# Performance work log

Hardware: AMD Instinct MI355X
Metric: run time of the kernel (lower is better)

## Reference

```python
import jax, jax.numpy as jnp
import numpy as np
import math

D_MODEL = 768
NUM_HEADS = 12
SPARSITY = 0.7


def setup_inputs() -> dict:
    key = jax.random.key(0)
    ks = jax.random.split(key, 9)
    B, S, D = 2, 2048, D_MODEL
    scale = 1.0 / math.sqrt(D)  # xavier-ish
    inp = {
        "x": jax.random.normal(ks[0], (B, S, D), dtype=jnp.float32),
        "Wq": jax.random.normal(ks[1], (D, D), dtype=jnp.float32) * scale,
        "bq": jnp.zeros((D,), dtype=jnp.float32),
        "Wk": jax.random.normal(ks[2], (D, D), dtype=jnp.float32) * scale,
        "bk": jnp.zeros((D,), dtype=jnp.float32),
        "Wv": jax.random.normal(ks[3], (D, D), dtype=jnp.float32) * scale,
        "bv": jnp.zeros((D,), dtype=jnp.float32),
        "Wo": jax.random.normal(ks[4], (D, D), dtype=jnp.float32) * scale,
        "bo": jnp.zeros((D,), dtype=jnp.float32),
    }
    return inp


def reference(x, Wq, bq, Wk, bk, Wv, bv, Wo, bo):
    B, S, D = x.shape
    H = NUM_HEADS
    hd = D // H
    k_keep = max(1, int((1.0 - SPARSITY) * S))

    # projections (nn.Linear: x @ W.T + b), split into heads -> [B,H,S,hd]
    q = (x @ Wq.T + bq).reshape(B, S, H, hd).transpose(0, 2, 1, 3)
    k = (x @ Wk.T + bk).reshape(B, S, H, hd).transpose(0, 2, 1, 3)
    v = (x @ Wv.T + bv).reshape(B, S, H, hd).transpose(0, 2, 1, 3)

    # dense scores [B,H,S,S]
    scores = jnp.einsum("bhqd,bhkd->bhqk", q, k) / math.sqrt(hd)

    # per-row top-k sparsification (training path of the torch module)
    _, topk_idx = jax.lax.top_k(scores, k_keep)  # [B,H,S,k]
    bi = jnp.arange(B)[:, None, None, None]
    hi = jnp.arange(H)[None, :, None, None]
    si = jnp.arange(S)[None, None, :, None]
    keep = jnp.zeros(scores.shape, dtype=bool).at[bi, hi, si, topk_idx].set(True)
    scores = jnp.where(keep, scores, jnp.float32(-1e9))

    attn = jax.nn.softmax(scores, axis=-1)
    out = jnp.einsum("bhqk,bhkd->bhqd", attn, v)  # [B,H,S,hd]
    out = out.transpose(0, 2, 1, 3).reshape(B, S, D)
    return out @ Wo.T + bo
```

## Files before the change

kernel.cpp:

```cpp
#include <hip/hip_runtime.h>
#include <math.h>

#define B_ 2
#define S_ 2048
#define D_ 768
#define H_ 12
#define HD_ 64
#define KKEEP 614
#define M_ (B_*S_)
#define KD_ 768
#define SRW 2072

typedef __attribute__((ext_vector_type(8))) short bf8;
typedef __attribute__((ext_vector_type(4))) float f4;

__device__ __forceinline__ unsigned short f2bf(float f) {
    unsigned u = __float_as_uint(f);
    u += 0x7FFF + ((u >> 16) & 1);
    return (unsigned short)(u >> 16);
}
__device__ __forceinline__ float bf2f(unsigned short h) {
    return __uint_as_float((unsigned)h << 16);
}
__device__ __forceinline__ unsigned f2ord16(float f) {
    unsigned u = __float_as_uint(f);
    unsigned o32 = u ^ ((unsigned)((int)u >> 31) | 0x80000000u);
    return (o32 + 0x7FFFu + ((o32 >> 16) & 1u)) >> 16;
}
__device__ __forceinline__ float ord16_to_f(unsigned o16) {
    unsigned o = o16 << 16;
    unsigned mask = 0x80000000u | ~(unsigned)((int)o >> 31);
    return __uint_as_float((o ^ mask) & 0xFFFF0000u);
}

__global__ void split_kernel(const float* __restrict__ src,
                             unsigned short* __restrict__ hi,
                             unsigned short* __restrict__ lo, int n) {
    int i = blockIdx.x * blockDim.x + threadIdx.x;
    if (i >= n) return;
    float f = src[i];
    unsigned short h = f2bf(f);
    hi[i] = h;
    lo[i] = f2bf(f - bf2f(h));
}

__global__ void split_w_kernel(const float* __restrict__ w0, const float* __restrict__ w1,
                               const float* __restrict__ w2, const float* __restrict__ w3,
                               unsigned short* __restrict__ hi,
                               unsigned short* __restrict__ lo) {
    const int which = blockIdx.y;
    const float* src = which == 0 ? w0 : (which == 1 ? w1 : (which == 2 ? w2 : w3));
    int i = blockIdx.x * blockDim.x + threadIdx.x;
    size_t o = (size_t)which * (D_ * D_) + i;
    float f = src[i];
    unsigned short h = f2bf(f);
    hi[o] = h;
    lo[o] = f2bf(f - bf2f(h));
}

__global__ __launch_bounds__(256)
void gemm_qkv(const unsigned short* __restrict__ Ahi, const unsigned short* __restrict__ Alo,
              const unsigned short* __restrict__ Wch, const unsigned short* __restrict__ Wcl,
              const float* __restrict__ bq, const float* __restrict__ bk,
              const float* __restrict__ bv,
              unsigned short* __restrict__ Qh, unsigned short* __restrict__ Ql,
              unsigned short* __restrict__ Kh, unsigned short* __restrict__ Vth) {
    __shared__ unsigned short Ah[128][32], Al[128][32], Bh[64][32], Bl[64][32];
    const int bm = blockIdx.x * 128, bnG = blockIdx.y * 64;
    const int which = blockIdx.y / 12;
    const int bn = bnG - which * 768;
    const float* bias = which == 0 ? bq : (which == 1 ? bk : bv);
    const int tid = threadIdx.x, lane = tid & 63, wave = tid >> 6;
    const int col = lane & 15, quad = lane >> 4;

    f4 acc[2][4];
#pragma unroll
    for (int mi = 0; mi < 2; ++mi)
#pragma unroll
        for (int ni = 0; ni < 4; ++ni) { f4 z = {0.f,0.f,0.f,0.f}; acc[mi][ni] = z; }

    for (int kt = 0; kt < KD_; kt += 32) {
        __syncthreads();
#pragma unroll
        for (int c = 0; c < 2; ++c) {
            int idx = c * 256 + tid;
            int row = idx >> 2, ko = (idx & 3) * 8;
            *(uint4*)&Ah[row][ko] = *(const uint4*)&Ahi[(size_t)(bm + row) * KD_ + kt + ko];
            *(uint4*)&Al[row][ko] = *(const uint4*)&Alo[(size_t)(bm + row) * KD_ + kt + ko];
        }
        {
            int row = tid >> 2, ko = (tid & 3) * 8;
            *(uint4*)&Bh[row][ko] = *(const uint4*)&Wch[(size_t)(bnG + row) * KD_ + kt + ko];
            *(uint4*)&Bl[row][ko] = *(const uint4*)&Wcl[(size_t)(bnG + row) * KD_ + kt + ko];
        }
        __syncthreads();

        bf8 af[2][2], wf[4][2];
#pragma unroll
        for (int mi = 0; mi < 2; ++mi) {
            int r = wave * 32 + mi * 16 + col;
            af[mi][0] = *(const bf8*)&Ah[r][quad * 8];
            af[mi][1] = *(const bf8*)&Al[r][quad * 8];
        }
#pragma unroll
        for (int ni = 0; ni < 4; ++ni) {
            int r = ni * 16 + col;
            wf[ni][0] = *(const bf8*)&Bh[r][quad * 8];
            wf[ni][1] = *(const bf8*)&Bl[r][quad * 8];
        }
#pragma unroll
        for (int mi = 0; mi < 2; ++mi)
#pragma unroll
            for (int ni = 0; ni < 4; ++ni) {
                acc[mi][ni] = __builtin_amdgcn_mfma_f32_16x16x32_bf16(af[mi][0], wf[ni][0], acc[mi][ni], 0, 0, 0);
                acc[mi][ni] = __builtin_amdgcn_mfma_f32_16x16x32_bf16(af[mi][1], wf[ni][0], acc[mi][ni], 0, 0, 0);
                acc[mi][ni] = __builtin_amdgcn_mfma_f32_16x16x32_bf16(af[mi][0], wf[ni][1], acc[mi][ni], 0, 0, 0);
            }
    }

    float bvv[4];
#pragma unroll
    for (int ni = 0; ni < 4; ++ni) bvv[ni] = bias[bn + ni * 16 + col];
#pragma unroll
    for (int mi = 0; mi < 2; ++mi)
#pragma unroll
        for (int ni = 0; ni < 4; ++ni)
#pragma unroll
            for (int r = 0; r < 4; ++r) {
                int m = bm + wave * 32 + mi * 16 + quad * 4 + r;
                int n = bn + ni * 16 + col;
                float v = acc[mi][ni][r] + bvv[ni];
                if (which == 0) v *= 0.125f;
                int b = m >> 11, s = m & 2047, h = n >> 6, d = n & 63;
                unsigned short hh = f2bf(v);
                if (which == 0) {
                    size_t idx = (((size_t)b * H_ + h) * S_ + s) * HD_ + d;
                    Qh[idx] = hh;
                    Ql[idx] = f2bf(v - bf2f(hh));
                } else if (which == 1) {
                    Kh[(((size_t)b * H_ + h) * S_ + s) * HD_ + d] = hh;
                } else {
                    Vth[(((size_t)b * H_ + h) * HD_ + d) * S_ + s] = hh;
                }
            }
}

__global__ __launch_bounds__(256)
void gemm_o(const unsigned short* __restrict__ Ahi, const unsigned short* __restrict__ Alo,
            const unsigned short* __restrict__ Whi, const unsigned short* __restrict__ Wlo,
            const float* __restrict__ bias, float* __restrict__ outf) {
    __shared__ unsigned short Ah[128][32], Al[128][32], Bh[64][32], Bl[64][32];
    const int bm = blockIdx.x * 128, bn = blockIdx.y * 64;
    const int tid = threadIdx.x, lane = tid & 63, wave = tid >> 6;
    const int col = lane & 15, quad = lane >> 4;

    f4 acc[2][4];
#pragma unroll
    for (int mi = 0; mi < 2; ++mi)
#pragma unroll
        for (int ni = 0; ni < 4; ++ni) { f4 z = {0.f,0.f,0.f,0.f}; acc[mi][ni] = z; }

    for (int kt = 0; kt < KD_; kt += 32) {
        __syncthreads();
#pragma unroll
        for (int c = 0; c < 2; ++c) {
            int idx = c * 256 + tid;
            int row = idx >> 2, ko = (idx & 3) * 8;
            *(uint4*)&Ah[row][ko] = *(const uint4*)&Ahi[(size_t)(bm + row) * KD_ + kt + ko];
            *(uint4*)&Al[row][ko] = *(const uint4*)&Alo[(size_t)(bm + row) * KD_ + kt + ko];
        }
        {
            int row = tid >> 2, ko = (tid & 3) * 8;
            *(uint4*)&Bh[row][ko] = *(const uint4*)&Whi[(size_t)(bn + row) * KD_ + kt + ko];
            *(uint4*)&Bl[row][ko] = *(const uint4*)&Wlo[(size_t)(bn + row) * KD_ + kt + ko];
        }
        __syncthreads();

        bf8 af[2][2], wf[4][2];
#pragma unroll
        for (int mi = 0; mi < 2; ++mi) {
            int r = wave * 32 + mi * 16 + col;
            af[mi][0] = *(const bf8*)&Ah[r][quad * 8];
            af[mi][1] = *(const bf8*)&Al[r][quad * 8];
        }
#pragma unroll
        for (int ni = 0; ni < 4; ++ni) {
            int r = ni * 16 + col;
            wf[ni][0] = *(const bf8*)&Bh[r][quad * 8];
            wf[ni][1] = *(const bf8*)&Bl[r][quad * 8];
        }
#pragma unroll
        for (int mi = 0; mi < 2; ++mi)
#pragma unroll
            for (int ni = 0; ni < 4; ++ni) {
                acc[mi][ni] = __builtin_amdgcn_mfma_f32_16x16x32_bf16(af[mi][0], wf[ni][0], acc[mi][ni], 0, 0, 0);
                acc[mi][ni] = __builtin_amdgcn_mfma_f32_16x16x32_bf16(af[mi][1], wf[ni][0], acc[mi][ni], 0, 0, 0);
                acc[mi][ni] = __builtin_amdgcn_mfma_f32_16x16x32_bf16(af[mi][0], wf[ni][1], acc[mi][ni], 0, 0, 0);
            }
    }

    float bvv[4];
#pragma unroll
    for (int ni = 0; ni < 4; ++ni) bvv[ni] = bias[bn + ni * 16 + col];
#pragma unroll
    for (int mi = 0; mi < 2; ++mi)
#pragma unroll
        for (int ni = 0; ni < 4; ++ni)
#pragma unroll
            for (int r = 0; r < 4; ++r) {
                int m = bm + wave * 32 + mi * 16 + quad * 4 + r;
                int n = bn + ni * 16 + col;
                outf[(size_t)m * D_ + n] = acc[mi][ni][r] + bvv[ni];
            }
}

__global__ __launch_bounds__(1024, 8)
void attn_kernel(const unsigned short* __restrict__ Qhi, const unsigned short* __restrict__ Qlo,
                 const unsigned short* __restrict__ Khi,
                 const unsigned short* __restrict__ Vthi,
                 unsigned short* __restrict__ AOhi, unsigned short* __restrict__ AOlo) {
    const int bid = blockIdx.x;
    const int xcd = bid & 7, sub = (bid >> 3) % 3, tile = bid / 24;
    const int bh = xcd * 3 + sub;
    const int b = bh / H_, h = bh % H_;
    const int q0 = tile * 16;
    const int tid = threadIdx.x, lane = tid & 63, wave = tid >> 6;
    const int col = lane & 15, quad = lane >> 4;

    __shared__ __align__(16) unsigned char arena[16 * 4144];
    unsigned short* scB = (unsigned short*)arena;
    float (*osum)[16][64] = (float (*)[16][64])arena;
    __shared__ float linv[16];

    const size_t qbase = ((size_t)bh * S_ + q0 + col) * HD_;
    bf8 qh0 = *(const bf8*)&Qhi[qbase + quad * 8];
    bf8 qh1 = *(const bf8*)&Qhi[qbase + 32 + quad * 8];
    bf8 ql0 = *(const bf8*)&Qlo[qbase + quad * 8];
    bf8 ql1 = *(const bf8*)&Qlo[qbase + 32 + quad * 8];

    const size_t kbb = (size_t)bh * S_ * HD_;
#pragma unroll 1
    for (int t = 0; t < 8; ++t) {
        const size_t kr = kbb + (size_t)(wave * 128 + t * 16 + col) * HD_;
        bf8 kh0 = *(const bf8*)&Khi[kr + quad * 8];
        bf8 kh1 = *(const bf8*)&Khi[kr + 32 + quad * 8];
        f4 a = {0.f, 0.f, 0.f, 0.f};
        a = __builtin_amdgcn_mfma_f32_16x16x32_bf16(qh0, kh0, a, 0, 0, 0);
        a = __builtin_amdgcn_mfma_f32_16x16x32_bf16(qh1, kh1, a, 0, 0, 0);
        a = __builtin_amdgcn_mfma_f32_16x16x32_bf16(ql0, kh0, a, 0, 0, 0);
        a = __builtin_amdgcn_mfma_f32_16x16x32_bf16(ql1, kh1, a, 0, 0, 0);
#pragma unroll
        for (int r = 0; r < 4; ++r)
            scB[(quad * 4 + r) * SRW + wave * 128 + t * 16 + col] =
                (unsigned short)f2ord16(a[r]);
    }
    __syncthreads();

    unsigned* rowp = (unsigned*)(arena + wave * 4144);
    unsigned kv[16], kvs[16];
#pragma unroll
    for (int j = 0; j < 16; ++j) kv[j] = rowp[lane + 64 * j];
#pragma unroll
    for (int j = 0; j < 16; ++j) kvs[j] = kv[j] << 16;

    unsigned Mhi = 0, Mlo = 0;
#pragma unroll
    for (int j = 0; j < 16; ++j) {
        Mhi = kv[j]  > Mhi ? kv[j]  : Mhi;
        Mlo = kvs[j] > Mlo ? kvs[j] : Mlo;
    }
    unsigned mo = (Mhi >> 16) > (Mlo >> 16) ? (Mhi >> 16) : (Mlo >> 16);
#pragma unroll
    for (int off = 1; off < 64; off <<= 1) {
        unsigned v = __shfl_xor((int)mo, off, 64);
        mo = mo > v ? mo : v;
    }
    const float m = ord16_to_f(mo);

    unsigned T = 0;
#pragma unroll 1
    for (int bit = 15; bit >= 0; --bit) {
        unsigned candh = (T | (1u << bit)) << 16;
        int cnt = 0;
#pragma unroll
        for (int j = 0; j < 16; ++j) {
            cnt += __popcll(__ballot(kv[j]  >= candh));
            cnt += __popcll(__ballot(kvs[j] >= candh));
        }
        if (cnt >= KKEEP) T |= (1u << bit);
    }

    float ls = 0.f;
#pragma unroll 1
    for (int j = 0; j < 16; ++j) {
        unsigned lo16 = kv[j] & 0xFFFFu;
        unsigned hi16 = kv[j] >> 16;
        float wl = __expf(ord16_to_f(lo16) - m);
        float wh = __expf(ord16_to_f(hi16) - m);
        wl = (lo16 >= T) ? wl : 0.f;
        wh = (hi16 >= T) ? wh : 0.f;
        ls += wl + wh;
        rowp[lane + 64 * j] = (unsigned)f2bf(wl) | ((unsigned)f2bf(wh) << 16);
    }
#pragma unroll
    for (int off = 1; off < 64; off <<= 1) ls += __shfl_xor(ls, off, 64);
    if (lane == 0) linv[wave] = 1.f / ls;
    __syncthreads();

    f4 od[4];
#pragma unroll
    for (int dt = 0; dt < 4; ++dt) { f4 z = {0.f,0.f,0.f,0.f}; od[dt] = z; }
    const size_t vbb = (size_t)bh * HD_ * S_;
#pragma unroll 1
    for (int c = 0; c < 4; ++c) {
        bf8 ph = *(const bf8*)&scB[col * SRW + wave * 128 + c * 32 + quad * 8];
        const size_t sbase = (size_t)(wave * 128 + c * 32 + quad * 8);
#pragma unroll
        for (int dt = 0; dt < 4; ++dt) {
            bf8 vh = *(const bf8*)&Vthi[vbb + (size_t)(dt * 16 + col) * S_ + sbase];
            od[dt] = __builtin_amdgcn_mfma_f32_16x16x32_bf16(ph, vh, od[dt], 0, 0, 0);
        }
    }
    __syncthreads();
#pragma unroll
    for (int dt = 0; dt < 4; ++dt)
#pragma unroll
        for (int r = 0; r < 4; ++r)
            osum[wave][quad * 4 + r][dt * 16 + col] = od[dt][r];
    __syncthreads();

    {
        int q = tid >> 6, d = tid & 63;
        float s = 0.f;
#pragma unroll
        for (int w = 0; w < 16; ++w) s += osum[w][q][d];
        s *= linv[q];
        size_t idx = ((size_t)b * S_ + q0 + q) * D_ + h * HD_ + d;
        unsigned short hh = f2bf(s);
        AOhi[idx] = hh;
        AOlo[idx] = f2bf(s - bf2f(hh));
    }
}

extern "C" void kernel_launch(void* const* d_in, const int* in_sizes, int n_in,
                              void* d_out, int out_size, void* d_ws, size_t ws_size,
                              hipStream_t stream) {
    const float* x  = (const float*)d_in[0];
    const float* Wq = (const float*)d_in[1];
    const float* bq = (const float*)d_in[2];
    const float* Wk = (const float*)d_in[3];
    const float* bk = (const float*)d_in[4];
    const float* Wv = (const float*)d_in[5];
    const float* bv = (const float*)d_in[6];
    const float* Wo = (const float*)d_in[7];
    const float* bo = (const float*)d_in[8];
    float* out = (float*)d_out;

    const size_t NP = (size_t)M_ * D_;
    const size_t NW = (size_t)D_ * D_;
    unsigned short* p = (unsigned short*)d_ws;
    unsigned short* xhi = p;  p += NP;
    unsigned short* xlo = p;  p += NP;
    unsigned short* Wch = p;  p += 4 * NW;
    unsigned short* Wcl = p;  p += 4 * NW;
    unsigned short* Qh  = p;  p += NP;  unsigned short* Ql  = p;  p += NP;
    unsigned short* Kh  = p;  p += NP;
    unsigned short* Vth = p;  p += NP;
    unsigned short* AOh = xhi;
    unsigned short* AOl = xlo;

    split_kernel<<<(int)(NP / 256), 256, 0, stream>>>(x, xhi, xlo, (int)NP);
    {
        dim3 gw((unsigned)(NW / 256), 4);
        split_w_kernel<<<gw, 256, 0, stream>>>(Wq, Wk, Wv, Wo, Wch, Wcl);
    }

    {
        dim3 g(M_ / 128, 36);
        gemm_qkv<<<g, 256, 0, stream>>>(xhi, xlo, Wch, Wcl, bq, bk, bv,
                                        Qh, Ql, Kh, Vth);
    }

    attn_kernel<<<(S_ / 16) * B_ * H_, 1024, 0, stream>>>(Qh, Ql, Kh, Vth, AOh, AOl);

    {
        dim3 g(M_ / 128, D_ / 64);
        gemm_o<<<g, 256, 0, stream>>>(AOh, AOl, Wch + 3 * NW, Wcl + 3 * NW, bo, out);
    }
}
```

Measured before the change: 433.4 us.

## Enlarge projection GEMM tiles to 128x128 and load tiles directly into LDS

```diff
diff --git a/kernel.cpp b/kernel.cpp
--- a/kernel.cpp
+++ b/kernel.cpp
@@ -31,6 +31,13 @@
     unsigned o = o16 << 16;
     unsigned mask = 0x80000000u | ~(unsigned)((int)o >> 31);
     return __uint_as_float((o ^ mask) & 0xFFFF0000u);
+}
+
+__device__ __forceinline__ void gload16(const unsigned short* g, unsigned short* l) {
+    __builtin_amdgcn_global_load_lds(
+        (const __attribute__((address_space(1))) unsigned int*)(const void*)g,
+        (__attribute__((address_space(3))) unsigned int*)(void*)l,
+        16, 0, 0);
 }
 
 __global__ void split_kernel(const float* __restrict__ src,
@@ -65,17 +72,18 @@
               const float* __restrict__ bv,
               unsigned short* __restrict__ Qh, unsigned short* __restrict__ Ql,
               unsigned short* __restrict__ Kh, unsigned short* __restrict__ Vth) {
-    __shared__ unsigned short Ah[128][32], Al[128][32], Bh[64][32], Bl[64][32];
-    const int bm = blockIdx.x * 128, bnG = blockIdx.y * 64;
-    const int which = blockIdx.y / 12;
-    const int bn = bnG - which * 768;
+    __shared__ unsigned short Ah[128][32], Al[128][32], Bh[128][32], Bl[128][32];
+    const int bm = blockIdx.x * 128, bnG = blockIdx.y * 128;
+    const int which = blockIdx.y / 6;
+    const int bnl = bnG - which * 768;
     const float* bias = which == 0 ? bq : (which == 1 ? bk : bv);
     const int tid = threadIdx.x, lane = tid & 63, wave = tid >> 6;
     const int col = lane & 15, quad = lane >> 4;
-
-    f4 acc[2][4];
-#pragma unroll
-    for (int mi = 0; mi < 2; ++mi)
+    const int wr = wave >> 1, wc = wave & 1;
+
+    f4 acc[4][4];
+#pragma unroll
+    for (int mi = 0; mi < 4; ++mi)
 #pragma unroll
         for (int ni = 0; ni < 4; ++ni) { f4 z = {0.f,0.f,0.f,0.f}; acc[mi][ni] = z; }
 
@@ -85,31 +93,30 @@
         for (int c = 0; c < 2; ++c) {
             int idx = c * 256 + tid;
             int row = idx >> 2, ko = (idx & 3) * 8;
-            *(uint4*)&Ah[row][ko] = *(const uint4*)&Ahi[(size_t)(bm + row) * KD_ + kt + ko];
-            *(uint4*)&Al[row][ko] = *(const uint4*)&Alo[(size_t)(bm + row) * KD_ + kt + ko];
-        }
-        {
-            int row = tid >> 2, ko = (tid & 3) * 8;
-            *(uint4*)&Bh[row][ko] = *(const uint4*)&Wch[(size_t)(bnG + row) * KD_ + kt + ko];
-            *(uint4*)&Bl[row][ko] = *(const uint4*)&Wcl[(size_t)(bnG + row) * KD_ + kt + ko];
+            size_t ga = (size_t)(bm + row) * KD_ + kt + ko;
+            size_t gb = (size_t)(bnG + row) * KD_ + kt + ko;
+            gload16(&Ahi[ga], &Ah[row][ko]);
+            gload16(&Alo[ga], &Al[row][ko]);
+            gload16(&Wch[gb], &Bh[row][ko]);
+            gload16(&Wcl[gb], &Bl[row][ko]);
         }
         __syncthreads();
 
-        bf8 af[2][2], wf[4][2];
-#pragma unroll
-        for (int mi = 0; mi < 2; ++mi) {
-            int r = wave * 32 + mi * 16 + col;
+        bf8 af[4][2], wf[4][2];
+#pragma unroll
+        for (int mi = 0; mi < 4; ++mi) {
+            int r = wr * 64 + mi * 16 + col;
             af[mi][0] = *(const bf8*)&Ah[r][quad * 8];
             af[mi][1] = *(const bf8*)&Al[r][quad * 8];
         }
 #pragma unroll
         for (int ni = 0; ni < 4; ++ni) {
-            int r = ni * 16 + col;
+            int r = wc * 64 + ni * 16 + col;
             wf[ni][0] = *(const bf8*)&Bh[r][quad * 8];
             wf[ni][1] = *(const bf8*)&Bl[r][quad * 8];
         }
 #pragma unroll
-        for (int mi = 0; mi < 2; ++mi)
+        for (int mi = 0; mi < 4; ++mi)
 #pragma unroll
             for (int ni = 0; ni < 4; ++ni) {
                 acc[mi][ni] = __builtin_amdgcn_mfma_f32_16x16x32_bf16(af[mi][0], wf[ni][0], acc[mi][ni], 0, 0, 0);
@@ -120,15 +127,15 @@
 
     float bvv[4];
 #pragma unroll
-    for (int ni = 0; ni < 4; ++ni) bvv[ni] = bias[bn + ni * 16 + col];
-#pragma unroll
-    for (int mi = 0; mi < 2; ++mi)
+    for (int ni = 0; ni < 4; ++ni) bvv[ni] = bias[bnl + wc * 64 + ni * 16 + col];
+#pragma unroll
+    for (int mi = 0; mi < 4; ++mi)
 #pragma unroll
         for (int ni = 0; ni < 4; ++ni)
 #pragma unroll
             for (int r = 0; r < 4; ++r) {
-                int m = bm + wave * 32 + mi * 16 + quad * 4 + r;
-                int n = bn + ni * 16 + col;
+                int m = bm + wr * 64 + mi * 16 + quad * 4 + r;
+                int n = bnl + wc * 64 + ni * 16 + col;
                 float v = acc[mi][ni][r] + bvv[ni];
                 if (which == 0) v *= 0.125f;
                 int b = m >> 11, s = m & 2047, h = n >> 6, d = n & 63;
@@ -149,14 +156,15 @@
 void gemm_o(const unsigned short* __restrict__ Ahi, const unsigned short* __restrict__ Alo,
             const unsigned short* __restrict__ Whi, const unsigned short* __restrict__ Wlo,
             const float* __restrict__ bias, float* __restrict__ outf) {
-    __shared__ unsigned short Ah[128][32], Al[128][32], Bh[64][32], Bl[64][32];
-    const int bm = blockIdx.x * 128, bn = blockIdx.y * 64;
+    __shared__ unsigned short Ah[128][32], Al[128][32], Bh[128][32], Bl[128][32];
+    const int bm = blockIdx.x * 128, bn = blockIdx.y * 128;
     const int tid = threadIdx.x, lane = tid & 63, wave = tid >> 6;
     const int col = lane & 15, quad = lane >> 4;
-
-    f4 acc[2][4];
-#pragma unroll
-    for (int mi = 0; mi < 2; ++mi)
+    const int wr = wave >> 1, wc = wave & 1;
+
+    f4 acc[4][4];
+#pragma unroll
+    for (int mi = 0; mi < 4; ++mi)
 #pragma unroll
         for (int ni = 0; ni < 4; ++ni) { f4 z = {0.f,0.f,0.f,0.f}; acc[mi][ni] = z; }
 
@@ -166,31 +174,30 @@
         for (int c = 0; c < 2; ++c) {
             int idx = c * 256 + tid;
             int row = idx >> 2, ko = (idx & 3) * 8;
-            *(uint4*)&Ah[row][ko] = *(const uint4*)&Ahi[(size_t)(bm + row) * KD_ + kt + ko];
-            *(uint4*)&Al[row][ko] = *(const uint4*)&Alo[(size_t)(bm + row) * KD_ + kt + ko];
-        }
-        {
-            int row = tid >> 2, ko = (tid & 3) * 8;
-            *(uint4*)&Bh[row][ko] = *(const uint4*)&Whi[(size_t)(bn + row) * KD_ + kt + ko];
-            *(uint4*)&Bl[row][ko] = *(const uint4*)&Wlo[(size_t)(bn + row) * KD_ + kt + ko];
+            size_t ga = (size_t)(bm + row) * KD_ + kt + ko;
+            size_t gb = (size_t)(bn + row) * KD_ + kt + ko;
+            gload16(&Ahi[ga], &Ah[row][ko]);
+            gload16(&Alo[ga], &Al[row][ko]);
+            gload16(&Whi[gb], &Bh[row][ko]);
+            gload16(&Wlo[gb], &Bl[row][ko]);
         }
         __syncthreads();
 
-        bf8 af[2][2], wf[4][2];
-#pragma unroll
-        for (int mi = 0; mi < 2; ++mi) {
-            int r = wave * 32 + mi * 16 + col;
+        bf8 af[4][2], wf[4][2];
+#pragma unroll
+        for (int mi = 0; mi < 4; ++mi) {
+            int r = wr * 64 + mi * 16 + col;
             af[mi][0] = *(const bf8*)&Ah[r][quad * 8];
             af[mi][1] = *(const bf8*)&Al[r][quad * 8];
         }
 #pragma unroll
         for (int ni = 0; ni < 4; ++ni) {
-            int r = ni * 16 + col;
+            int r = wc * 64 + ni * 16 + col;
             wf[ni][0] = *(const bf8*)&Bh[r][quad * 8];
             wf[ni][1] = *(const bf8*)&Bl[r][quad * 8];
         }
 #pragma unroll
-        for (int mi = 0; mi < 2; ++mi)
+        for (int mi = 0; mi < 4; ++mi)
 #pragma unroll
             for (int ni = 0; ni < 4; ++ni) {
                 acc[mi][ni] = __builtin_amdgcn_mfma_f32_16x16x32_bf16(af[mi][0], wf[ni][0], acc[mi][ni], 0, 0, 0);
@@ -201,15 +208,15 @@
 
     float bvv[4];
 #pragma unroll
-    for (int ni = 0; ni < 4; ++ni) bvv[ni] = bias[bn + ni * 16 + col];
-#pragma unroll
-    for (int mi = 0; mi < 2; ++mi)
+    for (int ni = 0; ni < 4; ++ni) bvv[ni] = bias[bn + wc * 64 + ni * 16 + col];
+#pragma unroll
+    for (int mi = 0; mi < 4; ++mi)
 #pragma unroll
         for (int ni = 0; ni < 4; ++ni)
 #pragma unroll
             for (int r = 0; r < 4; ++r) {
-                int m = bm + wave * 32 + mi * 16 + quad * 4 + r;
-                int n = bn + ni * 16 + col;
+                int m = bm + wr * 64 + mi * 16 + quad * 4 + r;
+                int n = bn + wc * 64 + ni * 16 + col;
                 outf[(size_t)m * D_ + n] = acc[mi][ni][r] + bvv[ni];
             }
 }
@@ -376,7 +383,7 @@
     }
 
     {
-        dim3 g(M_ / 128, 36);
+        dim3 g(M_ / 128, 18);
         gemm_qkv<<<g, 256, 0, stream>>>(xhi, xlo, Wch, Wcl, bq, bk, bv,
                                         Qh, Ql, Kh, Vth);
     }
@@ -384,7 +391,7 @@
     attn_kernel<<<(S_ / 16) * B_ * H_, 1024, 0, stream>>>(Qh, Ql, Kh, Vth, AOh, AOl);
 
     {
-        dim3 g(M_ / 128, D_ / 64);
+        dim3 g(M_ / 128, D_ / 128);
         gemm_o<<<g, 256, 0, stream>>>(AOh, AOl, Wch + 3 * NW, Wcl + 3 * NW, bo, out);
     }
 }
```

Result: slower. 447.5 us (+3.2%).

## Replace bitwise top-k threshold search with interpolation/bisection, fold log2e into Q scale

Applied to the files above, without the earlier changes.

```diff
diff --git a/kernel.cpp b/kernel.cpp
--- a/kernel.cpp
+++ b/kernel.cpp
@@ -130,7 +130,7 @@
                 int m = bm + wave * 32 + mi * 16 + quad * 4 + r;
                 int n = bn + ni * 16 + col;
                 float v = acc[mi][ni][r] + bvv[ni];
-                if (which == 0) v *= 0.125f;
+                if (which == 0) v *= 0.18033688f;
                 int b = m >> 11, s = m & 2047, h = n >> 6, d = n & 63;
                 unsigned short hh = f2bf(v);
                 if (which == 0) {
@@ -239,7 +239,7 @@
     bf8 ql1 = *(const bf8*)&Qlo[qbase + 32 + quad * 8];
 
     const size_t kbb = (size_t)bh * S_ * HD_;
-#pragma unroll 1
+#pragma unroll 2
     for (int t = 0; t < 8; ++t) {
         const size_t kr = kbb + (size_t)(wave * 128 + t * 16 + col) * HD_;
         bf8 kh0 = *(const bf8*)&Khi[kr + quad * 8];
@@ -277,17 +277,33 @@
     }
     const float m = ord16_to_f(mo);
 
-    unsigned T = 0;
-#pragma unroll 1
-    for (int bit = 15; bit >= 0; --bit) {
-        unsigned candh = (T | (1u << bit)) << 16;
+    unsigned lo = 0, hi = mo + 1;
+    int cnt_lo = 2048, cnt_hi = 0;
+    unsigned T;
+    unsigned probe = (mo > 0x200u) ? (mo - 0x200u) : 1u;
+    int iter = 0;
+    while (true) {
+        unsigned candh = probe << 16;
         int cnt = 0;
 #pragma unroll
         for (int j = 0; j < 16; ++j) {
             cnt += __popcll(__ballot(kv[j]  >= candh));
             cnt += __popcll(__ballot(kvs[j] >= candh));
         }
-        if (cnt >= KKEEP) T |= (1u << bit);
+        if (cnt == KKEEP) { T = probe; break; }
+        if (cnt > KKEEP) { lo = probe; cnt_lo = cnt; }
+        else             { hi = probe; cnt_hi = cnt; }
+        if (hi - lo <= 1) { T = lo; break; }
+        ++iter;
+        if (iter & 1) {
+            probe = (lo + hi) >> 1;
+        } else {
+            float f = (float)(cnt_lo - KKEEP) / (float)(cnt_lo - cnt_hi);
+            unsigned step = (unsigned)((float)(hi - lo) * f);
+            probe = lo + step;
+            if (probe <= lo) probe = lo + 1;
+            if (probe >= hi) probe = hi - 1;
+        }
     }
 
     float ls = 0.f;
@@ -295,8 +311,8 @@
     for (int j = 0; j < 16; ++j) {
         unsigned lo16 = kv[j] & 0xFFFFu;
         unsigned hi16 = kv[j] >> 16;
-        float wl = __expf(ord16_to_f(lo16) - m);
-        float wh = __expf(ord16_to_f(hi16) - m);
+        float wl = __builtin_amdgcn_exp2f(ord16_to_f(lo16) - m);
+        float wh = __builtin_amdgcn_exp2f(ord16_to_f(hi16) - m);
         wl = (lo16 >= T) ? wl : 0.f;
         wh = (hi16 >= T) ? wh : 0.f;
         ls += wl + wh;
```

New measurement: 407.6 us. 6.0% less time.
